# Optimization experiments

Hardware: AMD Instinct MI355X
Metric: run time of the kernel (lower is better)

Reference implementation:

```python
import jax, jax.numpy as jnp
from jax import lax
import numpy as np

SEQ = 1024
VOCAB = 50000
EMB = 300
CAS_V, CAS_D = 8, 50
POS_V, POS_D = 48, 50
IN_DIM = EMB + CAS_D + POS_D  # 400
H = 512
T = 13  # num_classes / CRF tags


def setup_inputs() -> dict:
    key = jax.random.key(0)
    ks = jax.random.split(key, 16)
    s = lambda k, shape, sc=0.05: jax.random.normal(k, shape, dtype=jnp.float32) * sc
    return {
        "x": jax.random.randint(ks[0], (SEQ,), 0, VOCAB),
        "casing": jax.random.randint(ks[1], (SEQ,), 0, CAS_V),
        "pos": jax.random.randint(ks[2], (SEQ,), 0, POS_V),
        "h0": jnp.zeros((2, H), dtype=jnp.float32),
        "c0": jnp.zeros((2, H), dtype=jnp.float32),
        "W_emb": s(ks[3], (VOCAB, EMB)),
        "W_cas": s(ks[4], (CAS_V, CAS_D)),
        "W_pos": s(ks[5], (POS_V, POS_D)),
        "Wx_f": s(ks[6], (IN_DIM, 4 * H)),
        "Wh_f": s(ks[7], (H, 4 * H)),
        "b_f": jnp.zeros((4 * H,), dtype=jnp.float32),
        "Wx_b": s(ks[8], (IN_DIM, 4 * H)),
        "Wh_b": s(ks[9], (H, 4 * H)),
        "b_b": jnp.zeros((4 * H,), dtype=jnp.float32),
        "W_out": s(ks[10], (2 * H, T)),
        "b_out": jnp.zeros((T,), dtype=jnp.float32),
        "trans": s(ks[11], (T, T), 0.1),
        "start_trans": s(ks[12], (T,), 0.1),
        "end_trans": s(ks[13], (T,), 0.1),
    }


def _lstm_dir(feat, Wx, Wh, b, h0, c0, reverse):
    # feat: [L, IN_DIM]; precompute input projection for all steps
    pre = feat @ Wx + b  # [L, 4H]

    def step(carry, p):
        h, c = carry
        z = p + h @ Wh
        i, f, g, o = jnp.split(z, 4, axis=-1)
        c = jax.nn.sigmoid(f) * c + jax.nn.sigmoid(i) * jnp.tanh(g)
        h = jax.nn.sigmoid(o) * jnp.tanh(c)
        return (h, c), h

    _, hs = lax.scan(step, (h0, c0), pre, reverse=reverse)
    return hs  # [L, H]


def _viterbi(em, trans, start_trans, end_trans):
    # em: [L, T] emission (log) scores; max-plus DP
    score0 = start_trans + em[0]

    def fwd(score, e):
        total = score[:, None] + trans  # [T, T]: prev -> next
        best = jnp.max(total, axis=0) + e
        idx = jnp.argmax(total, axis=0)
        return best, idx

    final, hist = lax.scan(fwd, score0, em[1:])  # hist: [L-1, T]
    final = final + end_trans
    last = jnp.argmax(final)

    def back(tag, idx_row):
        return idx_row[tag], tag

    first, rest = lax.scan(back, last, hist, reverse=True)
    return jnp.concatenate([first[None], rest])  # [L] int


def reference(x, casing, pos, h0, c0, W_emb, W_cas, W_pos, Wx_f, Wh_f, b_f,
              Wx_b, Wh_b, b_b, W_out, b_out, trans, start_trans, end_trans):
    # AWD-LSTM encode (eval mode: dropout identity)
    feat = jnp.concatenate([W_emb[x], W_cas[casing], W_pos[pos]], axis=-1)  # [L, 400]
    hf = _lstm_dir(feat, Wx_f, Wh_f, b_f, h0[0], c0[0], reverse=False)
    hb = _lstm_dir(feat, Wx_b, Wh_b, b_b, h0[1], c0[1], reverse=True)
    o = jnp.concatenate([hf, hb], axis=-1) @ W_out + b_out  # [L, T]
    tag_scores = jax.nn.log_softmax(o, axis=1)
    path = _viterbi(tag_scores, trans, start_trans, end_trans)
    return tag_scores, path
```

## Files before the change

### kernel.cpp

```cpp
#include <hip/hip_runtime.h>
#include <hip/hip_bf16.h>
#include <math.h>

#define SEQ 1024
#define HID 512
#define FOURH 2048
#define IND 400
#define NT 13

#define LSTM_WGS 64
#define NGEMM 256
#define JPW 16
#define WCOLS 64
#define TAG_INVALID 0xFFFFFFFFu

__device__ __forceinline__ float bf2f(unsigned short u) {
    union { unsigned u32; float f; } v;
    v.u32 = ((unsigned)u) << 16;
    return v.f;
}

__device__ __forceinline__ unsigned short f2bf(float f) {
    union { float f; unsigned u; } v;
    v.f = f;
    unsigned u = v.u;
    unsigned rounding = 0x7FFFu + ((u >> 16) & 1u);
    u += rounding;
    return (unsigned short)(u >> 16);
}

__device__ __forceinline__ float ldf(const void* p, size_t i, int isf32) {
    return isf32 ? ((const float*)p)[i] : bf2f(((const unsigned short*)p)[i]);
}

__device__ __forceinline__ float fsigm(float x) {
    return __builtin_amdgcn_rcpf(1.f + __builtin_amdgcn_exp2f(-1.44269504f * x));
}
__device__ __forceinline__ float ftanhf(float x) {
    return 1.f - 2.f * __builtin_amdgcn_rcpf(__builtin_amdgcn_exp2f(2.88539008f * x) + 1.f);
}
__device__ __forceinline__ float satz(float z) { return fminf(fmaxf(z, -60.f), 60.f); }

__global__ __launch_bounds__(64) void detect_kernel(const unsigned short* __restrict__ w,
                                                    int* __restrict__ flag,
                                                    unsigned* __restrict__ vcnt,
                                                    unsigned* __restrict__ flags) {
    int lane = threadIdx.x;
    int cnt = 0;
    for (int i = 0; i < 4; ++i) {
        unsigned short u = w[2 * (lane * 4 + i)];
        int e = (u >> 7) & 0xFF;
        if (e >= 90 && e < 127) cnt++;
    }
#pragma unroll
    for (int off = 32; off >= 1; off >>= 1) cnt += __shfl_xor(cnt, off, 64);
    if (lane == 0) *flag = (cnt < 128) ? 1 : 0;
    if (lane == 1) *vcnt = 0;
    flags[lane] = 0;
}

__global__ __launch_bounds__(512, 2) void fused_kernel(
        const int* __restrict__ x, const int* __restrict__ cas, const int* __restrict__ pos,
        const void* __restrict__ W_emb, const void* __restrict__ W_cas, const void* __restrict__ W_pos,
        const void* __restrict__ Wx_f, const void* __restrict__ b_f,
        const void* __restrict__ Wx_b, const void* __restrict__ b_b,
        const void* __restrict__ Wh_f, const void* __restrict__ Wh_b,
        const void* __restrict__ h0, const void* __restrict__ c0,
        unsigned long long* __restrict__ preu, float* __restrict__ hsout,
        unsigned long long* hbuf, const int* __restrict__ dflag,
        unsigned* __restrict__ flags) {
    __shared__ float smem[12800 + 96];
    const int isf32 = *dflag;
    const int tid = threadIdx.x;
    const int b = blockIdx.x;

    if (b >= LSTM_WGS) {
        const int e = b - LSTM_WGS;
        const int gdir = e & 1;
        const int rest = e >> 1;
        const int bx = rest & 3;
        const int byi = rest >> 2;
        const int by = (byi & 1) ? (31 - (byi >> 1)) : (byi >> 1);
        const void* Wx = gdir ? Wx_b : Wx_f;
        const void* bb = gdir ? b_b : b_f;
        const int r0 = by * 32;
        const int col = bx * 512 + tid;
        float* ftile = smem;
        int* idxs = (int*)&smem[12800];

        if (tid < 32)       idxs[tid] = x[r0 + tid];
        else if (tid < 64)  idxs[tid] = cas[r0 + tid - 32];
        else if (tid < 96)  idxs[tid] = pos[r0 + tid - 64];
        __syncthreads();

        for (int idx = tid; idx < 32 * IND; idx += 512) {
            int r = idx / IND;
            int el = idx - r * IND;
            float v;
            if (el < 300)      v = ldf(W_emb, (size_t)idxs[r] * 300 + el, isf32);
            else if (el < 350) v = ldf(W_cas, (size_t)idxs[32 + r] * 50 + (el - 300), isf32);
            else               v = ldf(W_pos, (size_t)idxs[64 + r] * 50 + (el - 350), isf32);
            ftile[idx] = v;
        }
        __syncthreads();

        float acc[32];
        float bias = ldf(bb, col, isf32);
#pragma unroll
        for (int r = 0; r < 32; ++r) acc[r] = bias;

        if (isf32) {
            const float* W = (const float*)Wx;
            for (int kk = 0; kk < 100; ++kk) {
                int k = kk * 4;
                float w0 = W[(size_t)(k + 0) * FOURH + col];
                float w1 = W[(size_t)(k + 1) * FOURH + col];
                float w2 = W[(size_t)(k + 2) * FOURH + col];
                float w3 = W[(size_t)(k + 3) * FOURH + col];
#pragma unroll
                for (int r = 0; r < 32; ++r) {
                    float4 f = *(const float4*)&ftile[r * IND + k];
                    acc[r] += f.x * w0 + f.y * w1 + f.z * w2 + f.w * w3;
                }
            }
        } else {
            const unsigned short* W = (const unsigned short*)Wx;
            for (int kk = 0; kk < 100; ++kk) {
                int k = kk * 4;
                float w0 = bf2f(W[(size_t)(k + 0) * FOURH + col]);
                float w1 = bf2f(W[(size_t)(k + 1) * FOURH + col]);
                float w2 = bf2f(W[(size_t)(k + 2) * FOURH + col]);
                float w3 = bf2f(W[(size_t)(k + 3) * FOURH + col]);
#pragma unroll
                for (int r = 0; r < 32; ++r) {
                    float4 f = *(const float4*)&ftile[r * IND + k];
                    acc[r] += f.x * w0 + f.y * w1 + f.z * w2 + f.w * w3;
                }
            }
        }

        unsigned long long* dst = preu + (size_t)gdir * SEQ * (FOURH / 4);
        for (int r = 0; r < 32; ++r) {
            unsigned long long w = ((unsigned long long)f2bf(acc[r])) << (16 * (tid & 3));
            w |= __shfl_xor(w, 1, 64);
            w |= __shfl_xor(w, 2, 64);
            if ((tid & 3) == 0)
                __hip_atomic_store(&dst[(size_t)(r0 + r) * 512 + (col >> 2)], w,
                                   __ATOMIC_RELAXED, __HIP_MEMORY_SCOPE_AGENT);
        }
        asm volatile("s_waitcnt vmcnt(0)" ::: "memory");
        __syncthreads();
        if (tid == 0) atomicAdd(&flags[gdir * 32 + by], 1u);
        return;
    }

    float* redp = smem;
    const int dir = b & 1;
    const int g = b >> 1;
    const int j0 = g * JPW;

    const void* Wh = dir ? Wh_b : Wh_f;
    const unsigned long long* preu_d = preu + (size_t)dir * SEQ * 512;
    float* hso = hsout + (size_t)dir * SEQ * HID;
    unsigned long long* hb_d  = hbuf + dir * 2 * HID;
    unsigned long long* hb2_d = hbuf + 4096 + dir * 2 * HID;

    const int seg  = tid >> 6;
    const int col  = tid & 63;
    const int unit = col & 15;
    const int gate = col >> 4;
    const int gcol = gate * HID + j0 + unit;
    const int redoff = seg * WCOLS + unit * 4 + gate;

    const int isep  = (tid < 64);
    const int eunit = tid >> 2;
    const int egate = tid & 3;
    const int ispub = isep && (egate == 0);
    const int sub   = eunit & 3;
    const int widx  = egate * 128 + ((j0 + eunit) >> 2);

    float4 w0, w1, w2, w3, w4, w5, w6, w7, w8, w9, w10, w11, w12, w13, w14, w15;
    if (isf32) {
        const float* wp = (const float*)Wh + (size_t)(seg * 64) * FOURH + gcol;
#define LDW(i) w##i = make_float4(wp[(size_t)(4*i+0)*FOURH], wp[(size_t)(4*i+1)*FOURH], \
                                  wp[(size_t)(4*i+2)*FOURH], wp[(size_t)(4*i+3)*FOURH])
        LDW(0); LDW(1); LDW(2); LDW(3); LDW(4); LDW(5); LDW(6); LDW(7);
        LDW(8); LDW(9); LDW(10); LDW(11); LDW(12); LDW(13); LDW(14); LDW(15);
#undef LDW
    } else {
        const unsigned short* wp = (const unsigned short*)Wh + (size_t)(seg * 64) * FOURH + gcol;
#define LDW(i) w##i = make_float4(bf2f(wp[(size_t)(4*i+0)*FOURH]), bf2f(wp[(size_t)(4*i+1)*FOURH]), \
                                  bf2f(wp[(size_t)(4*i+2)*FOURH]), bf2f(wp[(size_t)(4*i+3)*FOURH]))
        LDW(0); LDW(1); LDW(2); LDW(3); LDW(4); LDW(5); LDW(6); LDW(7);
        LDW(8); LDW(9); LDW(10); LDW(11); LDW(12); LDW(13); LDW(14); LDW(15);
#undef LDW
    }

    float creg = 0.f;
    unsigned long long znw = 0;
    int curby = dir ? 31 : 0;
    if (isep) {
        if (ispub) {
            creg = ldf(c0, dir * HID + j0 + eunit, isf32);
            float h0v = ldf(h0, dir * HID + j0 + eunit, isf32);
            unsigned long long wv = (unsigned long long)__float_as_uint(h0v);
            unsigned long long iv = ((unsigned long long)TAG_INVALID << 32);
            __hip_atomic_store(&hb_d[j0 + eunit],        wv, __ATOMIC_RELAXED, __HIP_MEMORY_SCOPE_AGENT);
            __hip_atomic_store(&hb2_d[j0 + eunit],       wv, __ATOMIC_RELAXED, __HIP_MEMORY_SCOPE_AGENT);
            __hip_atomic_store(&hb_d[HID + j0 + eunit],  iv, __ATOMIC_RELAXED, __HIP_MEMORY_SCOPE_AGENT);
            __hip_atomic_store(&hb2_d[HID + j0 + eunit], iv, __ATOMIC_RELAXED, __HIP_MEMORY_SCOPE_AGENT);
        }
        {
            const unsigned* fp = &flags[dir * 32 + curby];
            while (__hip_atomic_load(fp, __ATOMIC_RELAXED, __HIP_MEMORY_SCOPE_AGENT) < 4u) {}
        }
        int t0 = dir ? (SEQ - 1) : 0;
        znw = __hip_atomic_load(&preu_d[(size_t)t0 * 512 + widx],
                                __ATOMIC_RELAXED, __HIP_MEMORY_SCOPE_AGENT);
    }
    __syncthreads();

    for (int s = 0; s < SEQ; ++s) {
        const int t = dir ? (SEQ - 1 - s) : s;

        unsigned hu;
        {
            const unsigned long long* A = &hb_d[(s & 1) * HID + tid];
            const unsigned long long* B = &hb2_d[(s & 1) * HID + tid];
            const unsigned expect = (unsigned)s;
            unsigned long long va = __hip_atomic_load(A, __ATOMIC_RELAXED, __HIP_MEMORY_SCOPE_AGENT);
            unsigned long long vb = __hip_atomic_load(B, __ATOMIC_RELAXED, __HIP_MEMORY_SCOPE_AGENT);
            for (;;) {
                if ((unsigned)(va >> 32) == expect) { hu = (unsigned)va; break; }
                va = __hip_atomic_load(A, __ATOMIC_RELAXED, __HIP_MEMORY_SCOPE_AGENT);
                if ((unsigned)(vb >> 32) == expect) { hu = (unsigned)vb; break; }
                vb = __hip_atomic_load(B, __ATOMIC_RELAXED, __HIP_MEMORY_SCOPE_AGENT);
            }
        }

        float zc = 0.f;
        if (isep) {
            zc = bf2f((unsigned short)(znw >> (16 * sub)));
            if (s + 1 < SEQ) {
                int tn = dir ? (SEQ - 2 - s) : (s + 1);
                int byn = tn >> 5;
                if (byn != curby) {
                    const unsigned* fp = &flags[dir * 32 + byn];
                    while (__hip_atomic_load(fp, __ATOMIC_RELAXED, __HIP_MEMORY_SCOPE_AGENT) < 4u) {}
                    curby = byn;
                }
                znw = __hip_atomic_load(&preu_d[(size_t)tn * 512 + widx],
                                        __ATOMIC_RELAXED, __HIP_MEMORY_SCOPE_AGENT);
            }
        }

        float a0 = 0.f, a1 = 0.f, a2 = 0.f, a3 = 0.f;
#define MACQ(i, A) { \
        float hx = __uint_as_float((unsigned)__builtin_amdgcn_readlane((int)hu, 4*i+0)); \
        float hy = __uint_as_float((unsigned)__builtin_amdgcn_readlane((int)hu, 4*i+1)); \
        float hz = __uint_as_float((unsigned)__builtin_amdgcn_readlane((int)hu, 4*i+2)); \
        float hw = __uint_as_float((unsigned)__builtin_amdgcn_readlane((int)hu, 4*i+3)); \
        A += hx * w##i.x + hy * w##i.y + hz * w##i.z + hw * w##i.w; }
        MACQ(0, a0)  MACQ(1, a1)  MACQ(2, a2)  MACQ(3, a3)
        MACQ(4, a0)  MACQ(5, a1)  MACQ(6, a2)  MACQ(7, a3)
        MACQ(8, a0)  MACQ(9, a1)  MACQ(10, a2) MACQ(11, a3)
        MACQ(12, a0) MACQ(13, a1) MACQ(14, a2) MACQ(15, a3)
#undef MACQ
        redp[(s & 1) * 512 + redoff] = (a0 + a1) + (a2 + a3);
        __syncthreads();

        if (isep) {
            const float* rp = &redp[(s & 1) * 512];
            float z = rp[0 * WCOLS + tid] + rp[1 * WCOLS + tid]
                    + rp[2 * WCOLS + tid] + rp[3 * WCOLS + tid]
                    + rp[4 * WCOLS + tid] + rp[5 * WCOLS + tid]
                    + rp[6 * WCOLS + tid] + rp[7 * WCOLS + tid];
            z = satz(z + zc);
            float vs = fsigm(z);
            float vt = ftanhf(z);
            float v = (egate == 2) ? vt : vs;
            float x1 = __shfl_xor(v, 1, 64);
            float x2 = __shfl_xor(v, 2, 64);
            float x3 = __shfl_xor(x1, 2, 64);
            if (ispub) {
                float ig = v, fg = x1, gg = x2, og = x3;
                float cnew = fg * creg + ig * gg;
                creg = cnew;
                float hnew = og * ftanhf(satz(cnew));
                unsigned long long w = ((unsigned long long)(unsigned)(s + 1) << 32)
                                     | (unsigned long long)__float_as_uint(hnew);
                const int par = (s + 1) & 1;
                __hip_atomic_store(&hb_d[par * HID + j0 + eunit], w,
                                   __ATOMIC_RELAXED, __HIP_MEMORY_SCOPE_AGENT);
                __hip_atomic_store(&hb2_d[par * HID + j0 + eunit], w,
                                   __ATOMIC_RELAXED, __HIP_MEMORY_SCOPE_AGENT);
                hso[(size_t)t * HID + j0 + eunit] = hnew;
            }
        }
    }
}

__global__ __launch_bounds__(64) void outproj_kernel(const float* __restrict__ hsout,
        const void* __restrict__ W_out, const void* __restrict__ b_out,
        float* __restrict__ out_scores,
        const void* __restrict__ trans, const void* __restrict__ strans,
        const void* __restrict__ etrans, float* __restrict__ out_path,
        unsigned* __restrict__ vcnt, const int* __restrict__ dflag) {
    __shared__ unsigned char hist[SEQ][NT];
    const int isf32 = *dflag;
    int t = blockIdx.x;
    int lane = threadIdx.x;
    const float* hf = hsout + (size_t)t * HID;
    const float* hb = hsout + (size_t)SEQ * HID + (size_t)t * HID;
    float acc[NT];
#pragma unroll
    for (int j = 0; j < NT; ++j) acc[j] = 0.f;
    for (int k = lane; k < HID; k += 64) {
        float a = hf[k], b2 = hb[k];
#pragma unroll
        for (int j = 0; j < NT; ++j)
            acc[j] += a * ldf(W_out, (size_t)k * NT + j, isf32)
                    + b2 * ldf(W_out, (size_t)(HID + k) * NT + j, isf32);
    }
#pragma unroll
    for (int off = 32; off >= 1; off >>= 1) {
#pragma unroll
        for (int j = 0; j < NT; ++j) acc[j] += __shfl_xor(acc[j], off, 64);
    }
    float o[NT];
    float m = -1e30f;
#pragma unroll
    for (int j = 0; j < NT; ++j) { o[j] = acc[j] + ldf(b_out, j, isf32); m = fmaxf(m, o[j]); }
    float lse = 0.f;
#pragma unroll
    for (int j = 0; j < NT; ++j) lse += expf(o[j] - m);
    lse = m + logf(lse);
    if (lane < NT)
        __hip_atomic_store(&out_scores[t * NT + lane], o[lane] - lse,
                           __ATOMIC_RELAXED, __HIP_MEMORY_SCOPE_AGENT);
    __builtin_amdgcn_s_waitcnt(0);

    unsigned old = 0;
    if (lane == 0) old = atomicAdd(vcnt, 1u);
    old = __shfl(old, 0, 64);
    if (old != SEQ - 1) return;

    const float* em = out_scores;
    int j = lane < NT ? lane : 0;
    float tr[NT];
#pragma unroll
    for (int i = 0; i < NT; ++i) tr[i] = ldf(trans, i * NT + j, isf32);
#define EML(tt) __hip_atomic_load(&em[(size_t)(tt) * NT + j], __ATOMIC_RELAXED, __HIP_MEMORY_SCOPE_AGENT)
    float score = ldf(strans, j, isf32) + EML(0);
    float c0 = EML(1), c1 = EML(2), c2 = EML(3), c3 = EML(4),
          c4 = EML(5), c5 = EML(6), c6 = EML(7), c7 = EML(8);
#define VSTEP(PE, TT) { \
    float best = -1e30f; int arg = 0; \
    _Pragma("unroll") \
    for (int i = 0; i < NT; ++i) { \
        float si = __shfl(score, i, 64); \
        float cand = si + tr[i]; \
        if (cand > best) { best = cand; arg = i; } \
    } \
    if (lane < NT) hist[TT][lane] = (unsigned char)arg; \
    score = best + PE; }
    for (int tb = 1; tb < SEQ; tb += 8) {
        int nb = tb + 8;
        float n0 = 0.f, n1 = 0.f, n2 = 0.f, n3 = 0.f, n4 = 0.f, n5 = 0.f, n6 = 0.f, n7 = 0.f;
        if (nb + 0 < SEQ) n0 = EML(nb + 0);
        if (nb + 1 < SEQ) n1 = EML(nb + 1);
        if (nb + 2 < SEQ) n2 = EML(nb + 2);
        if (nb + 3 < SEQ) n3 = EML(nb + 3);
        if (nb + 4 < SEQ) n4 = EML(nb + 4);
        if (nb + 5 < SEQ) n5 = EML(nb + 5);
        if (nb + 6 < SEQ) n6 = EML(nb + 6);
        if (nb + 7 < SEQ) n7 = EML(nb + 7);
        VSTEP(c0, tb + 0)
        if (tb + 1 < SEQ) VSTEP(c1, tb + 1)
        if (tb + 2 < SEQ) VSTEP(c2, tb + 2)
        if (tb + 3 < SEQ) VSTEP(c3, tb + 3)
        if (tb + 4 < SEQ) VSTEP(c4, tb + 4)
        if (tb + 5 < SEQ) VSTEP(c5, tb + 5)
        if (tb + 6 < SEQ) VSTEP(c6, tb + 6)
        if (tb + 7 < SEQ) VSTEP(c7, tb + 7)
        c0 = n0; c1 = n1; c2 = n2; c3 = n3; c4 = n4; c5 = n5; c6 = n6; c7 = n7;
    }
#undef VSTEP
#undef EML
    score += ldf(etrans, j, isf32);
    float bmax = -1e30f;
    int last = 0;
#pragma unroll
    for (int i = 0; i < NT; ++i) {
        float si = __shfl(score, i, 64);
        if (si > bmax) { bmax = si; last = i; }
    }
    if (lane == 0) {
        int cur = last;
        out_path[SEQ - 1] = (float)cur;
        for (int tt = SEQ - 1; tt >= 1; --tt) {
            cur = hist[tt][cur];
            out_path[tt - 1] = (float)cur;
        }
    }
}

extern "C" void kernel_launch(void* const* d_in, const int* in_sizes, int n_in,
                              void* d_out, int out_size, void* d_ws, size_t ws_size,
                              hipStream_t stream) {
    const int* x      = (const int*)d_in[0];
    const int* casing = (const int*)d_in[1];
    const int* posi   = (const int*)d_in[2];
    const void* h0    = d_in[3];
    const void* c0    = d_in[4];
    const void* W_emb = d_in[5];
    const void* W_cas = d_in[6];
    const void* W_pos = d_in[7];
    const void* Wx_f  = d_in[8];
    const void* Wh_f  = d_in[9];
    const void* b_f   = d_in[10];
    const void* Wx_b  = d_in[11];
    const void* Wh_b  = d_in[12];
    const void* b_b   = d_in[13];
    const void* W_out = d_in[14];
    const void* b_out = d_in[15];
    const void* trans = d_in[16];
    const void* strans = d_in[17];
    const void* etrans = d_in[18];

    char* ws = (char*)d_ws;
    int* dflag          = (int*)(ws + 448);
    unsigned* vcnt      = (unsigned*)(ws + 456);
    unsigned long long* preu = (unsigned long long*)(ws + 512);
    float* hsout        = (float*)(ws + 512 + 8388608);
    unsigned long long* hbuf = (unsigned long long*)(ws + 512 + 8388608 + 4194304);
    unsigned* flags     = (unsigned*)(ws + 512 + 8388608 + 4194304 + 65536);

    float* out_scores = (float*)d_out;
    float* out_path   = out_scores + SEQ * NT;

    detect_kernel<<<1, 64, 0, stream>>>((const unsigned short*)W_emb, dflag, vcnt, flags);

    fused_kernel<<<LSTM_WGS + NGEMM, 512, 0, stream>>>(
        x, casing, posi, W_emb, W_cas, W_pos, Wx_f, b_f, Wx_b, b_b,
        Wh_f, Wh_b, h0, c0, preu, hsout, hbuf, dflag, flags);

    outproj_kernel<<<SEQ, 64, 0, stream>>>(hsout, W_out, b_out, out_scores,
                                           trans, strans, etrans, out_path, vcnt, dflag);
}
```

Baseline: 2.305 ms.

## Split critical first input-projection tile finer and reschedule GEMM tiles across fewer blocks

The GEMM workgroups that compute the LSTM input projection are restructured. The first row block each direction needs (row 0 forward, row 31 backward) is now split across 8 half-width workgroups so it finishes sooner and the recurrence can start earlier. The remaining tiles are spread over fewer workgroups, some handling two tiles in time order. The flag thresholds for the critical block change to match. This trades per-block GEMM efficiency and total GEMM parallelism for lower startup latency on the serial LSTM chain.

```diff
diff --git a/kernel.cpp b/kernel.cpp
--- a/kernel.cpp
+++ b/kernel.cpp
@@ -9,7 +9,7 @@
 #define NT 13
 
 #define LSTM_WGS 64
-#define NGEMM 256
+#define NGEMM 192
 #define JPW 16
 #define WCOLS 64
 #define TAG_INVALID 0xFFFFFFFFu
@@ -77,80 +77,158 @@
     if (b >= LSTM_WGS) {
         const int e = b - LSTM_WGS;
         const int gdir = e & 1;
-        const int rest = e >> 1;
-        const int bx = rest & 3;
-        const int byi = rest >> 2;
-        const int by = (byi & 1) ? (31 - (byi >> 1)) : (byi >> 1);
+        const int i = e >> 1;
         const void* Wx = gdir ? Wx_b : Wx_f;
         const void* bb = gdir ? b_b : b_f;
-        const int r0 = by * 32;
-        const int col = bx * 512 + tid;
+        unsigned long long* dst = preu + (size_t)gdir * SEQ * 512;
         float* ftile = smem;
         int* idxs = (int*)&smem[12800];
-
-        if (tid < 32)       idxs[tid] = x[r0 + tid];
-        else if (tid < 64)  idxs[tid] = cas[r0 + tid - 32];
-        else if (tid < 96)  idxs[tid] = pos[r0 + tid - 64];
-        __syncthreads();
-
-        for (int idx = tid; idx < 32 * IND; idx += 512) {
-            int r = idx / IND;
-            int el = idx - r * IND;
-            float v;
-            if (el < 300)      v = ldf(W_emb, (size_t)idxs[r] * 300 + el, isf32);
-            else if (el < 350) v = ldf(W_cas, (size_t)idxs[32 + r] * 50 + (el - 300), isf32);
-            else               v = ldf(W_pos, (size_t)idxs[64 + r] * 50 + (el - 350), isf32);
-            ftile[idx] = v;
-        }
-        __syncthreads();
-
-        float acc[32];
-        float bias = ldf(bb, col, isf32);
-#pragma unroll
-        for (int r = 0; r < 32; ++r) acc[r] = bias;
-
-        if (isf32) {
-            const float* W = (const float*)Wx;
-            for (int kk = 0; kk < 100; ++kk) {
-                int k = kk * 4;
-                float w0 = W[(size_t)(k + 0) * FOURH + col];
-                float w1 = W[(size_t)(k + 1) * FOURH + col];
-                float w2 = W[(size_t)(k + 2) * FOURH + col];
-                float w3 = W[(size_t)(k + 3) * FOURH + col];
-#pragma unroll
-                for (int r = 0; r < 32; ++r) {
-                    float4 f = *(const float4*)&ftile[r * IND + k];
-                    acc[r] += f.x * w0 + f.y * w1 + f.z * w2 + f.w * w3;
+        const int critby = gdir ? 31 : 0;
+
+        if (i < 8) {
+            const int r0 = critby * 32;
+            const int c  = tid & 255;
+            const int rg = tid >> 8;
+            const int col = i * 256 + c;
+
+            if (tid < 32)       idxs[tid] = x[r0 + tid];
+            else if (tid < 64)  idxs[tid] = cas[r0 + tid - 32];
+            else if (tid < 96)  idxs[tid] = pos[r0 + tid - 64];
+            __syncthreads();
+            for (int idx = tid; idx < 32 * IND; idx += 512) {
+                int r = idx / IND;
+                int el = idx - r * IND;
+                float v;
+                if (el < 300)      v = ldf(W_emb, (size_t)idxs[r] * 300 + el, isf32);
+                else if (el < 350) v = ldf(W_cas, (size_t)idxs[32 + r] * 50 + (el - 300), isf32);
+                else               v = ldf(W_pos, (size_t)idxs[64 + r] * 50 + (el - 350), isf32);
+                ftile[idx] = v;
+            }
+            __syncthreads();
+
+            float acc[16];
+            float bias = ldf(bb, col, isf32);
+#pragma unroll
+            for (int r = 0; r < 16; ++r) acc[r] = bias;
+
+            if (isf32) {
+                const float* W = (const float*)Wx;
+                for (int kk = 0; kk < 100; ++kk) {
+                    int k = kk * 4;
+                    float w0 = W[(size_t)(k + 0) * FOURH + col];
+                    float w1 = W[(size_t)(k + 1) * FOURH + col];
+                    float w2 = W[(size_t)(k + 2) * FOURH + col];
+                    float w3 = W[(size_t)(k + 3) * FOURH + col];
+#pragma unroll
+                    for (int rr = 0; rr < 16; ++rr) {
+                        float4 f = *(const float4*)&ftile[(rg * 16 + rr) * IND + k];
+                        acc[rr] += f.x * w0 + f.y * w1 + f.z * w2 + f.w * w3;
+                    }
                 }
-            }
-        } else {
-            const unsigned short* W = (const unsigned short*)Wx;
-            for (int kk = 0; kk < 100; ++kk) {
-                int k = kk * 4;
-                float w0 = bf2f(W[(size_t)(k + 0) * FOURH + col]);
-                float w1 = bf2f(W[(size_t)(k + 1) * FOURH + col]);
-                float w2 = bf2f(W[(size_t)(k + 2) * FOURH + col]);
-                float w3 = bf2f(W[(size_t)(k + 3) * FOURH + col]);
-#pragma unroll
-                for (int r = 0; r < 32; ++r) {
-                    float4 f = *(const float4*)&ftile[r * IND + k];
-                    acc[r] += f.x * w0 + f.y * w1 + f.z * w2 + f.w * w3;
+            } else {
+                const unsigned short* W = (const unsigned short*)Wx;
+                for (int kk = 0; kk < 100; ++kk) {
+                    int k = kk * 4;
+                    float w0 = bf2f(W[(size_t)(k + 0) * FOURH + col]);
+                    float w1 = bf2f(W[(size_t)(k + 1) * FOURH + col]);
+                    float w2 = bf2f(W[(size_t)(k + 2) * FOURH + col]);
+                    float w3 = bf2f(W[(size_t)(k + 3) * FOURH + col]);
+#pragma unroll
+                    for (int rr = 0; rr < 16; ++rr) {
+                        float4 f = *(const float4*)&ftile[(rg * 16 + rr) * IND + k];
+                        acc[rr] += f.x * w0 + f.y * w1 + f.z * w2 + f.w * w3;
+                    }
                 }
             }
-        }
-
-        unsigned long long* dst = preu + (size_t)gdir * SEQ * (FOURH / 4);
-        for (int r = 0; r < 32; ++r) {
-            unsigned long long w = ((unsigned long long)f2bf(acc[r])) << (16 * (tid & 3));
-            w |= __shfl_xor(w, 1, 64);
-            w |= __shfl_xor(w, 2, 64);
-            if ((tid & 3) == 0)
-                __hip_atomic_store(&dst[(size_t)(r0 + r) * 512 + (col >> 2)], w,
-                                   __ATOMIC_RELAXED, __HIP_MEMORY_SCOPE_AGENT);
-        }
-        asm volatile("s_waitcnt vmcnt(0)" ::: "memory");
-        __syncthreads();
-        if (tid == 0) atomicAdd(&flags[gdir * 32 + by], 1u);
+
+            for (int rr = 0; rr < 16; ++rr) {
+                int r = rg * 16 + rr;
+                unsigned long long w = ((unsigned long long)f2bf(acc[rr])) << (16 * (tid & 3));
+                w |= __shfl_xor(w, 1, 64);
+                w |= __shfl_xor(w, 2, 64);
+                if ((tid & 3) == 0)
+                    __hip_atomic_store(&dst[(size_t)(r0 + r) * 512 + (col >> 2)], w,
+                                       __ATOMIC_RELAXED, __HIP_MEMORY_SCOPE_AGENT);
+            }
+            asm volatile("s_waitcnt vmcnt(0)" ::: "memory");
+            __syncthreads();
+            if (tid == 0) atomicAdd(&flags[gdir * 32 + critby], 1u);
+            return;
+        }
+
+        const int j = i - 8;
+        const int q = j >> 2;
+        const int ntile = (j < 36) ? 2 : 1;
+        for (int ti = 0; ti < ntile; ++ti) {
+            const int by = (ti == 0) ? (gdir ? (30 - q) : (1 + q))
+                                     : (gdir ? (8 - q)  : (23 + q));
+            const int bx = j & 3;
+            const int r0 = by * 32;
+            const int col = bx * 512 + tid;
+
+            __syncthreads();
+            if (tid < 32)       idxs[tid] = x[r0 + tid];
+            else if (tid < 64)  idxs[tid] = cas[r0 + tid - 32];
+            else if (tid < 96)  idxs[tid] = pos[r0 + tid - 64];
+            __syncthreads();
+            for (int idx = tid; idx < 32 * IND; idx += 512) {
+                int r = idx / IND;
+                int el = idx - r * IND;
+                float v;
+                if (el < 300)      v = ldf(W_emb, (size_t)idxs[r] * 300 + el, isf32);
+                else if (el < 350) v = ldf(W_cas, (size_t)idxs[32 + r] * 50 + (el - 300), isf32);
+                else               v = ldf(W_pos, (size_t)idxs[64 + r] * 50 + (el - 350), isf32);
+                ftile[idx] = v;
+            }
+            __syncthreads();
+
+            float acc[32];
+            float bias = ldf(bb, col, isf32);
+#pragma unroll
+            for (int r = 0; r < 32; ++r) acc[r] = bias;
+
+            if (isf32) {
+                const float* W = (const float*)Wx;
+                for (int kk = 0; kk < 100; ++kk) {
+                    int k = kk * 4;
+                    float w0 = W[(size_t)(k + 0) * FOURH + col];
+                    float w1 = W[(size_t)(k + 1) * FOURH + col];
+                    float w2 = W[(size_t)(k + 2) * FOURH + col];
+                    float w3 = W[(size_t)(k + 3) * FOURH + col];
+#pragma unroll
+                    for (int r = 0; r < 32; ++r) {
+                        float4 f = *(const float4*)&ftile[r * IND + k];
+                        acc[r] += f.x * w0 + f.y * w1 + f.z * w2 + f.w * w3;
+                    }
+                }
+            } else {
+                const unsigned short* W = (const unsigned short*)Wx;
+                for (int kk = 0; kk < 100; ++kk) {
+                    int k = kk * 4;
+                    float w0 = bf2f(W[(size_t)(k + 0) * FOURH + col]);
+                    float w1 = bf2f(W[(size_t)(k + 1) * FOURH + col]);
+                    float w2 = bf2f(W[(size_t)(k + 2) * FOURH + col]);
+                    float w3 = bf2f(W[(size_t)(k + 3) * FOURH + col]);
+#pragma unroll
+                    for (int r = 0; r < 32; ++r) {
+                        float4 f = *(const float4*)&ftile[r * IND + k];
+                        acc[r] += f.x * w0 + f.y * w1 + f.z * w2 + f.w * w3;
+                    }
+                }
+            }
+
+            for (int r = 0; r < 32; ++r) {
+                unsigned long long w = ((unsigned long long)f2bf(acc[r])) << (16 * (tid & 3));
+                w |= __shfl_xor(w, 1, 64);
+                w |= __shfl_xor(w, 2, 64);
+                if ((tid & 3) == 0)
+                    __hip_atomic_store(&dst[(size_t)(r0 + r) * 512 + (col >> 2)], w,
+                                       __ATOMIC_RELAXED, __HIP_MEMORY_SCOPE_AGENT);
+            }
+            asm volatile("s_waitcnt vmcnt(0)" ::: "memory");
+            __syncthreads();
+            if (tid == 0) atomicAdd(&flags[gdir * 32 + by], 1u);
+        }
         return;
     }
 
@@ -158,6 +236,7 @@
     const int dir = b & 1;
     const int g = b >> 1;
     const int j0 = g * JPW;
+    const int critby = dir ? 31 : 0;
 
     const void* Wh = dir ? Wh_b : Wh_f;
     const unsigned long long* preu_d = preu + (size_t)dir * SEQ * 512;
@@ -198,7 +277,7 @@
 
     float creg = 0.f;
     unsigned long long znw = 0;
-    int curby = dir ? 31 : 0;
+    int curby = critby;
     if (isep) {
         if (ispub) {
             creg = ldf(c0, dir * HID + j0 + eunit, isf32);
@@ -212,7 +291,7 @@
         }
         {
             const unsigned* fp = &flags[dir * 32 + curby];
-            while (__hip_atomic_load(fp, __ATOMIC_RELAXED, __HIP_MEMORY_SCOPE_AGENT) < 4u) {}
+            while (__hip_atomic_load(fp, __ATOMIC_RELAXED, __HIP_MEMORY_SCOPE_AGENT) < 8u) {}
         }
         int t0 = dir ? (SEQ - 1) : 0;
         znw = __hip_atomic_load(&preu_d[(size_t)t0 * 512 + widx],
@@ -245,8 +324,9 @@
                 int tn = dir ? (SEQ - 2 - s) : (s + 1);
                 int byn = tn >> 5;
                 if (byn != curby) {
+                    const unsigned thr = (byn == critby) ? 8u : 4u;
                     const unsigned* fp = &flags[dir * 32 + byn];
-                    while (__hip_atomic_load(fp, __ATOMIC_RELAXED, __HIP_MEMORY_SCOPE_AGENT) < 4u) {}
+                    while (__hip_atomic_load(fp, __ATOMIC_RELAXED, __HIP_MEMORY_SCOPE_AGENT) < thr) {}
                     curby = byn;
                 }
                 znw = __hip_atomic_load(&preu_d[(size_t)tn * 512 + widx],
```

After: 2.260 ms. About the same (-1.9%).
